# Performance work log

Hardware: AMD Instinct MI355X
Metric: run time of the kernel (lower is better)

## Reference

```python
import jax, jax.numpy as jnp
import numpy as np

N = 50000
E = 800000
D = 64


def setup_inputs() -> dict:
    key = jax.random.key(0)
    ks = jax.random.split(key, 6)
    s = 1.0 / np.sqrt(D)
    return {
        "x": jax.random.normal(ks[0], (N, D), dtype=jnp.float32),
        "edge_index": jax.random.randint(ks[1], (2, E), 0, N, dtype=jnp.int64),
        "W_l1": jax.random.normal(ks[2], (D, D), dtype=jnp.float32) * s,
        "b_l1": jnp.zeros((D,), dtype=jnp.float32),
        "W_r1": jax.random.normal(ks[3], (D, D), dtype=jnp.float32) * s,
        "W_l2": jax.random.normal(ks[4], (D, D), dtype=jnp.float32) * s,
        "b_l2": jnp.zeros((D,), dtype=jnp.float32),
        "W_r2": jax.random.normal(ks[5], (D, D), dtype=jnp.float32) * s,
    }


def _sage_conv(x, src, dst, W_l, b_l, W_r):
    # PyG SAGEConv (aggr='mean'): out = lin_l(mean_{j in N(i)} x_j) + lin_r(x_i)
    msgs = x[src]                                   # [E, D] gather
    agg = jax.ops.segment_sum(msgs, dst, num_segments=N)          # [N, D]
    cnt = jax.ops.segment_sum(jnp.ones((src.shape[0],), x.dtype), dst,
                              num_segments=N)                      # [N]
    agg = agg / jnp.maximum(cnt, 1.0)[:, None]       # mean with deg>=1 guard
    return agg @ W_l.T + b_l + x @ W_r.T


def reference(x, edge_index, W_l1, b_l1, W_r1, W_l2, b_l2, W_r2):
    src, dst = edge_index[0], edge_index[1]
    h = jnp.tanh(_sage_conv(x, src, dst, W_l1, b_l1, W_r1))
    out = _sage_conv(h, src, dst, W_l2, b_l2, W_r2)
    return out
```

## Files before the change

kernel.cpp:

```cpp
#include <hip/hip_runtime.h>
#include <hip/hip_bf16.h>

#define D 64

typedef __attribute__((ext_vector_type(8))) short bf16x8;
typedef __attribute__((ext_vector_type(4))) float f32x4;

__device__ __forceinline__ float bf2f(unsigned short u) {
    return __uint_as_float(((unsigned)u) << 16);
}
__device__ __forceinline__ unsigned short f2bf(float f) {
    __hip_bfloat16 b = __float2bfloat16(f);
    return *(unsigned short*)&b;
}


__global__ void prep_k(const float* __restrict__ x, unsigned short* __restrict__ xbf,
                       const float* __restrict__ Wl1, const float* __restrict__ Wr1,
                       const float* __restrict__ Wl2, const float* __restrict__ Wr2,
                       unsigned short* __restrict__ Wbf,
                       int* __restrict__ cnt, int n4, int ncnt4) {
    int i = blockIdx.x * blockDim.x + threadIdx.x;
    if (i < n4) {
        float4 v = ((const float4*)x)[i];
        ushort4 u;
        u.x = f2bf(v.x); u.y = f2bf(v.y); u.z = f2bf(v.z); u.w = f2bf(v.w);
        ((ushort4*)xbf)[i] = u;
    }
    if (i < ncnt4) ((int4*)cnt)[i] = make_int4(0, 0, 0, 0);
    if (i < 4096) {
        Wbf[i]           = f2bf(Wl1[i]);
        Wbf[4096 + i]    = f2bf(Wr1[i]);
        Wbf[8192 + i]    = f2bf(Wl2[i]);
        Wbf[12288 + i]   = f2bf(Wr2[i]);
    }
}


__global__ void pos_k(const int* __restrict__ dst, int* __restrict__ cnt,
                      unsigned short* __restrict__ pos, int E) {
    int e0 = (blockIdx.x * blockDim.x + threadIdx.x) * 4;
    if (e0 + 4 <= E) {
        int4 d = *(const int4*)(dst + e0);
        int px = atomicAdd(&cnt[d.x], 1);
        int py = atomicAdd(&cnt[d.y], 1);
        int pz = atomicAdd(&cnt[d.z], 1);
        int pw = atomicAdd(&cnt[d.w], 1);
        *(ushort4*)(pos + e0) = make_ushort4((unsigned short)px, (unsigned short)py,
                                             (unsigned short)pz, (unsigned short)pw);
    } else {
        for (int e = e0; e < E; ++e)
            pos[e] = (unsigned short)atomicAdd(&cnt[dst[e]], 1);
    }
}

__global__ void scanA_k(const int* __restrict__ cnt, int* __restrict__ rowptrL,
                        int* __restrict__ bsum, int N) {
    __shared__ int tmp[256];
    int gid = blockIdx.x * 256 + threadIdx.x;
    int v = (gid < N) ? cnt[gid] : 0;
    tmp[threadIdx.x] = v;
    __syncthreads();
    for (int off = 1; off < 256; off <<= 1) {
        int t = (threadIdx.x >= off) ? tmp[threadIdx.x - off] : 0;
        __syncthreads();
        tmp[threadIdx.x] += t;
        __syncthreads();
    }
    if (gid < N) rowptrL[gid] = tmp[threadIdx.x] - v;
    if (threadIdx.x == 255) bsum[blockIdx.x] = tmp[255];
}

__global__ void scanB_k(int* __restrict__ bsum, int nb) {
    __shared__ int tmp[256];
    int v = (threadIdx.x < nb) ? bsum[threadIdx.x] : 0;
    tmp[threadIdx.x] = v;
    __syncthreads();
    for (int off = 1; off < 256; off <<= 1) {
        int t = (threadIdx.x >= off) ? tmp[threadIdx.x - off] : 0;
        __syncthreads();
        tmp[threadIdx.x] += t;
        __syncthreads();
    }
    if (threadIdx.x < nb) bsum[threadIdx.x] = tmp[threadIdx.x] - v;
}

__global__ void fill2_k(const int* __restrict__ src, const int* __restrict__ dst,
                        const unsigned short* __restrict__ pos,
                        const int* __restrict__ rowptrL, const int* __restrict__ bsum,
                        unsigned short* __restrict__ col, int E) {
    int e0 = (blockIdx.x * blockDim.x + threadIdx.x) * 4;
    if (e0 + 4 <= E) {
        int4 d = *(const int4*)(dst + e0);
        int4 s = *(const int4*)(src + e0);
        ushort4 p = *(const ushort4*)(pos + e0);
        col[rowptrL[d.x] + bsum[d.x >> 8] + p.x] = (unsigned short)s.x;
        col[rowptrL[d.y] + bsum[d.y >> 8] + p.y] = (unsigned short)s.y;
        col[rowptrL[d.z] + bsum[d.z >> 8] + p.z] = (unsigned short)s.z;
        col[rowptrL[d.w] + bsum[d.w >> 8] + p.w] = (unsigned short)s.w;
    } else {
        for (int e = e0; e < E; ++e)
            col[rowptrL[dst[e]] + bsum[dst[e] >> 8] + pos[e]] = (unsigned short)src[e];
    }
}


__device__ __forceinline__ float tanh_fast(float v) {
    float e = __expf(2.f * v);
    return 1.f - 2.f * __builtin_amdgcn_rcpf(e + 1.f);
}

template <int TANH>
__global__ __launch_bounds__(256) void layer_k(
    const unsigned short* __restrict__ xb,
    const int* __restrict__ rowptrL, const int* __restrict__ bsum,
    const unsigned short* __restrict__ col,
    const unsigned short* __restrict__ Wlb,
    const unsigned short* __restrict__ Wrb,
    const float* __restrict__ bias,
    float* __restrict__ outf, unsigned short* __restrict__ outb, int N, int E)
{
    __shared__ unsigned short sagg[16][72];
    const int tid = threadIdx.x;
    const int idx = tid & 15;
    const int nl  = tid >> 4;
    const int n0  = blockIdx.x * 16;
    const int n   = n0 + nl;

    if (n < N) {
        const int beg = rowptrL[n] + bsum[n >> 8];
        const int end = (n + 1 < N) ? (rowptrL[n + 1] + bsum[(n + 1) >> 8]) : E;
        float ax[8], ay[8], az[8], aw[8];
        #pragma unroll
        for (int s = 0; s < 8; ++s) { ax[s]=0.f; ay[s]=0.f; az[s]=0.f; aw[s]=0.f; }
        for (int j = beg; j < end; j += 8) {
            #pragma unroll
            for (int s = 0; s < 8; ++s) {
                int jj = j + s;
                float m = (jj < end) ? 1.f : 0.f;
                jj = (jj < end) ? jj : end - 1;
                int c = col[jj];
                ushort4 u = *(const ushort4*)(xb + (size_t)c * D + idx * 4);
                ax[s] = fmaf(m, bf2f(u.x), ax[s]);
                ay[s] = fmaf(m, bf2f(u.y), ay[s]);
                az[s] = fmaf(m, bf2f(u.z), az[s]);
                aw[s] = fmaf(m, bf2f(u.w), aw[s]);
            }
        }
        float sx = ((ax[0]+ax[1])+(ax[2]+ax[3]))+((ax[4]+ax[5])+(ax[6]+ax[7]));
        float sy = ((ay[0]+ay[1])+(ay[2]+ay[3]))+((ay[4]+ay[5])+(ay[6]+ay[7]));
        float sz = ((az[0]+az[1])+(az[2]+az[3]))+((az[4]+az[5])+(az[6]+az[7]));
        float sw = ((aw[0]+aw[1])+(aw[2]+aw[3]))+((aw[4]+aw[5])+(aw[6]+aw[7]));
        const float inv = 1.0f / fmaxf((float)(end - beg), 1.0f);
        ushort4 o;
        o.x = f2bf(sx*inv); o.y = f2bf(sy*inv); o.z = f2bf(sz*inv); o.w = f2bf(sw*inv);
        *(ushort4*)&sagg[nl][idx * 4] = o;
    } else {
        *(ushort4*)&sagg[nl][idx * 4] = make_ushort4(0, 0, 0, 0);
    }
    __syncthreads();

    const int lane = tid & 63;
    const int wid  = tid >> 6;
    const int fr   = lane & 15;
    const int k0   = (lane >> 4) * 8;
    const int f    = wid * 16 + fr;

    bf16x8 bl[2], br[2];
    {
        const unsigned short* pl = Wlb + f * 64 + k0;
        const unsigned short* pr = Wrb + f * 64 + k0;
        #pragma unroll
        for (int kc = 0; kc < 2; ++kc) {
            bl[kc] = *(const bf16x8*)(pl + kc * 32);
            br[kc] = *(const bf16x8*)(pr + kc * 32);
        }
    }
    float bv = bias[f];
    f32x4 acc = (f32x4){bv, bv, bv, bv};

    bf16x8 aa[2], axf[2];
    #pragma unroll
    for (int kc = 0; kc < 2; ++kc)
        aa[kc] = *(const bf16x8*)&sagg[fr][kc * 32 + k0];
    {
        const unsigned short* px = xb + (size_t)(n0 + fr) * D + k0;
        #pragma unroll
        for (int kc = 0; kc < 2; ++kc)
            axf[kc] = *(const bf16x8*)(px + kc * 32);
    }

    #pragma unroll
    for (int kc = 0; kc < 2; ++kc) {
        acc = __builtin_amdgcn_mfma_f32_16x16x32_bf16(aa[kc],  bl[kc], acc, 0, 0, 0);
        acc = __builtin_amdgcn_mfma_f32_16x16x32_bf16(axf[kc], br[kc], acc, 0, 0, 0);
    }

    const int rbase = n0 + (lane >> 4) * 4;
    #pragma unroll
    for (int r = 0; r < 4; ++r) {
        int node = rbase + r;
        if (node < N) {
            float v = acc[r];
            if (TANH) {
                v = tanh_fast(v);
                outb[(size_t)node * D + f] = f2bf(v);
            } else {
                outf[(size_t)node * D + f] = v;
            }
        }
    }
}


extern "C" void kernel_launch(void* const* d_in, const int* in_sizes, int n_in,
                              void* d_out, int out_size, void* d_ws, size_t ws_size,
                              hipStream_t stream) {
    const float* x   = (const float*)d_in[0];
    const int*   ei  = (const int*)d_in[1];
    const float* Wl1 = (const float*)d_in[2];
    const float* bl1 = (const float*)d_in[3];
    const float* Wr1 = (const float*)d_in[4];
    const float* Wl2 = (const float*)d_in[5];
    const float* bl2 = (const float*)d_in[6];
    const float* Wr2 = (const float*)d_in[7];

    const int N = in_sizes[0] / D;
    const int E = in_sizes[1] / 2;
    const int* srcI = ei;
    const int* dstI = ei + E;

    auto al = [](size_t v) { return (v + 255) & ~(size_t)255; };
    char* w = (char*)d_ws;
    size_t off = 0;
    int*            cnt     = (int*)(w + off);            off += al((size_t)N * 4);
    int*            rowptrL = (int*)(w + off);            off += al((size_t)N * 4);
    int*            bsum    = (int*)(w + off);            off += al(1024);
    unsigned short* colA    = (unsigned short*)(w + off); off += al((size_t)E * 2);
    unsigned short* pos     = (unsigned short*)(w + off); off += al((size_t)E * 2);
    unsigned short* xbf     = (unsigned short*)(w + off); off += al((size_t)N * D * 2);
    unsigned short* hbf     = (unsigned short*)(w + off); off += al((size_t)N * D * 2);
    unsigned short* Wbf     = (unsigned short*)(w + off); off += al((size_t)4 * D * D * 2);
    unsigned short* Wb_l1 = Wbf, *Wb_r1 = Wbf + D*D, *Wb_l2 = Wbf + 2*D*D, *Wb_r2 = Wbf + 3*D*D;

    float* out = (float*)d_out;

    const int NB  = (N + 255) / 256;
    const int EB4 = (E / 4 + 255) / 256;
    const int PB  = (N * D / 4 + 255) / 256;
    const int LB  = (N + 15) / 16;

    prep_k<<<PB, 256, 0, stream>>>(x, xbf, Wl1, Wr1, Wl2, Wr2, Wbf,
                                   cnt, N * D / 4, (N + 3) / 4);
    pos_k<<<EB4, 256, 0, stream>>>(dstI, cnt, pos, E);
    scanA_k<<<NB, 256, 0, stream>>>(cnt, rowptrL, bsum, N);
    scanB_k<<<1, 256, 0, stream>>>(bsum, NB);
    fill2_k<<<EB4, 256, 0, stream>>>(srcI, dstI, pos, rowptrL, bsum, colA, E);

    layer_k<1><<<LB, 256, 0, stream>>>(xbf, rowptrL, bsum, colA, Wb_l1, Wb_r1, bl1,
                                       nullptr, hbf, N, E);
    layer_k<0><<<LB, 256, 0, stream>>>(hbf, rowptrL, bsum, colA, Wb_l2, Wb_r2, bl2,
                                       out, nullptr, N, E);
}
```

Before: 121.2 us.

## Split feature columns into two half-tables and aggregate each in separate passes

Stores bf16 node features as two 32-column halves. A new kernel aggregates the first half into a buffer, and the layer kernel aggregates the second half and combines both before the MFMA linear step. Each gather pass then touches a 3.2 MB table instead of 6.4 MB, aiming for better cache hit rates on the random neighbor gathers. The cost is an extra kernel launch per layer, a second walk over the column indices, and an extra write and read of the half-aggregate. The N bounds checks were also dropped, which is safe only because N is a multiple of 16.

```diff
diff --git a/kernel.cpp b/kernel.cpp
--- a/kernel.cpp
+++ b/kernel.cpp
@@ -15,7 +15,8 @@
 }
 
 
-__global__ void prep_k(const float* __restrict__ x, unsigned short* __restrict__ xbf,
+__global__ void prep_k(const float* __restrict__ x,
+                       unsigned short* __restrict__ xbA, unsigned short* __restrict__ xbB,
                        const float* __restrict__ Wl1, const float* __restrict__ Wr1,
                        const float* __restrict__ Wl2, const float* __restrict__ Wr2,
                        unsigned short* __restrict__ Wbf,
@@ -23,9 +24,11 @@
     int i = blockIdx.x * blockDim.x + threadIdx.x;
     if (i < n4) {
         float4 v = ((const float4*)x)[i];
+        int n = i >> 4, q = i & 15;
         ushort4 u;
         u.x = f2bf(v.x); u.y = f2bf(v.y); u.z = f2bf(v.z); u.w = f2bf(v.w);
-        ((ushort4*)xbf)[i] = u;
+        if (q < 8) *(ushort4*)(xbA + (size_t)n * 32 + q * 4) = u;
+        else       *(ushort4*)(xbB + (size_t)n * 32 + (q - 8) * 4) = u;
     }
     if (i < ncnt4) ((int4*)cnt)[i] = make_int4(0, 0, 0, 0);
     if (i < 4096) {
@@ -105,59 +108,102 @@
 }
 
 
+__global__ __launch_bounds__(256) void aggA_k(
+    const unsigned short* __restrict__ xbA,
+    const int* __restrict__ rowptrL, const int* __restrict__ bsum,
+    const unsigned short* __restrict__ col,
+    unsigned short* __restrict__ aggbA, int N, int E)
+{
+    const int tid = threadIdx.x;
+    const int idx = tid & 7;
+    const int n   = blockIdx.x * 32 + (tid >> 3);
+    if (n >= N) return;
+    const int beg = rowptrL[n] + bsum[n >> 8];
+    const int end = (n + 1 < N) ? (rowptrL[n + 1] + bsum[(n + 1) >> 8]) : E;
+
+    float ax[8], ay[8], az[8], aw[8];
+    #pragma unroll
+    for (int s = 0; s < 8; ++s) { ax[s]=0.f; ay[s]=0.f; az[s]=0.f; aw[s]=0.f; }
+    for (int j = beg; j < end; j += 8) {
+        #pragma unroll
+        for (int s = 0; s < 8; ++s) {
+            int jj = j + s;
+            float m = (jj < end) ? 1.f : 0.f;
+            jj = (jj < end) ? jj : end - 1;
+            int c = col[jj];
+            ushort4 u = *(const ushort4*)(xbA + (size_t)c * 32 + idx * 4);
+            ax[s] = fmaf(m, bf2f(u.x), ax[s]);
+            ay[s] = fmaf(m, bf2f(u.y), ay[s]);
+            az[s] = fmaf(m, bf2f(u.z), az[s]);
+            aw[s] = fmaf(m, bf2f(u.w), aw[s]);
+        }
+    }
+    float sx = ((ax[0]+ax[1])+(ax[2]+ax[3]))+((ax[4]+ax[5])+(ax[6]+ax[7]));
+    float sy = ((ay[0]+ay[1])+(ay[2]+ay[3]))+((ay[4]+ay[5])+(ay[6]+ay[7]));
+    float sz = ((az[0]+az[1])+(az[2]+az[3]))+((az[4]+az[5])+(az[6]+az[7]));
+    float sw = ((aw[0]+aw[1])+(aw[2]+aw[3]))+((aw[4]+aw[5])+(aw[6]+aw[7]));
+    const float inv = 1.0f / fmaxf((float)(end - beg), 1.0f);
+    ushort4 o;
+    o.x = f2bf(sx*inv); o.y = f2bf(sy*inv); o.z = f2bf(sz*inv); o.w = f2bf(sw*inv);
+    *(ushort4*)(aggbA + (size_t)n * 32 + idx * 4) = o;
+}
+
+
 __device__ __forceinline__ float tanh_fast(float v) {
     float e = __expf(2.f * v);
     return 1.f - 2.f * __builtin_amdgcn_rcpf(e + 1.f);
 }
 
 template <int TANH>
-__global__ __launch_bounds__(256) void layer_k(
-    const unsigned short* __restrict__ xb,
+__global__ __launch_bounds__(256) void layerB_k(
+    const unsigned short* __restrict__ xbA,
+    const unsigned short* __restrict__ xbB,
+    const unsigned short* __restrict__ aggbA,
     const int* __restrict__ rowptrL, const int* __restrict__ bsum,
     const unsigned short* __restrict__ col,
     const unsigned short* __restrict__ Wlb,
     const unsigned short* __restrict__ Wrb,
     const float* __restrict__ bias,
-    float* __restrict__ outf, unsigned short* __restrict__ outb, int N, int E)
+    float* __restrict__ outf,
+    unsigned short* __restrict__ houtA,
+    unsigned short* __restrict__ houtB,
+    int N, int E)
 {
     __shared__ unsigned short sagg[16][72];
     const int tid = threadIdx.x;
+    const int n0  = blockIdx.x * 16;
+
+    ushort4 aA;
+    if (tid < 128) aA = *(const ushort4*)(aggbA + (size_t)(n0 + (tid >> 3)) * 32 + (tid & 7) * 4);
+
     const int idx = tid & 15;
     const int nl  = tid >> 4;
-    const int n0  = blockIdx.x * 16;
     const int n   = n0 + nl;
-
-    if (n < N) {
-        const int beg = rowptrL[n] + bsum[n >> 8];
-        const int end = (n + 1 < N) ? (rowptrL[n + 1] + bsum[(n + 1) >> 8]) : E;
-        float ax[8], ay[8], az[8], aw[8];
+    const int beg = rowptrL[n] + bsum[n >> 8];
+    const int end = (n + 1 < N) ? (rowptrL[n + 1] + bsum[(n + 1) >> 8]) : E;
+    float ax[8], ay[8];
+    #pragma unroll
+    for (int s = 0; s < 8; ++s) { ax[s] = 0.f; ay[s] = 0.f; }
+    for (int j = beg; j < end; j += 8) {
         #pragma unroll
-        for (int s = 0; s < 8; ++s) { ax[s]=0.f; ay[s]=0.f; az[s]=0.f; aw[s]=0.f; }
-        for (int j = beg; j < end; j += 8) {
-            #pragma unroll
-            for (int s = 0; s < 8; ++s) {
-                int jj = j + s;
-                float m = (jj < end) ? 1.f : 0.f;
-                jj = (jj < end) ? jj : end - 1;
-                int c = col[jj];
-                ushort4 u = *(const ushort4*)(xb + (size_t)c * D + idx * 4);
-                ax[s] = fmaf(m, bf2f(u.x), ax[s]);
-                ay[s] = fmaf(m, bf2f(u.y), ay[s]);
-                az[s] = fmaf(m, bf2f(u.z), az[s]);
-                aw[s] = fmaf(m, bf2f(u.w), aw[s]);
-            }
+        for (int s = 0; s < 8; ++s) {
+            int jj = j + s;
+            float m = (jj < end) ? 1.f : 0.f;
+            jj = (jj < end) ? jj : end - 1;
+            int c = col[jj];
+            ushort2 u = *(const ushort2*)(xbB + (size_t)c * 32 + idx * 2);
+            ax[s] = fmaf(m, bf2f(u.x), ax[s]);
+            ay[s] = fmaf(m, bf2f(u.y), ay[s]);
         }
-        float sx = ((ax[0]+ax[1])+(ax[2]+ax[3]))+((ax[4]+ax[5])+(ax[6]+ax[7]));
-        float sy = ((ay[0]+ay[1])+(ay[2]+ay[3]))+((ay[4]+ay[5])+(ay[6]+ay[7]));
-        float sz = ((az[0]+az[1])+(az[2]+az[3]))+((az[4]+az[5])+(az[6]+az[7]));
-        float sw = ((aw[0]+aw[1])+(aw[2]+aw[3]))+((aw[4]+aw[5])+(aw[6]+aw[7]));
-        const float inv = 1.0f / fmaxf((float)(end - beg), 1.0f);
-        ushort4 o;
-        o.x = f2bf(sx*inv); o.y = f2bf(sy*inv); o.z = f2bf(sz*inv); o.w = f2bf(sw*inv);
-        *(ushort4*)&sagg[nl][idx * 4] = o;
-    } else {
-        *(ushort4*)&sagg[nl][idx * 4] = make_ushort4(0, 0, 0, 0);
-    }
+    }
+    float sx = ((ax[0]+ax[1])+(ax[2]+ax[3]))+((ax[4]+ax[5])+(ax[6]+ax[7]));
+    float sy = ((ay[0]+ay[1])+(ay[2]+ay[3]))+((ay[4]+ay[5])+(ay[6]+ay[7]));
+    const float inv = 1.0f / fmaxf((float)(end - beg), 1.0f);
+    ushort2 ob;
+    ob.x = f2bf(sx * inv); ob.y = f2bf(sy * inv);
+
+    if (tid < 128) *(ushort4*)&sagg[tid >> 3][(tid & 7) * 4] = aA;
+    *(ushort2*)&sagg[nl][32 + idx * 2] = ob;
     __syncthreads();
 
     const int lane = tid & 63;
@@ -180,15 +226,10 @@
     f32x4 acc = (f32x4){bv, bv, bv, bv};
 
     bf16x8 aa[2], axf[2];
-    #pragma unroll
-    for (int kc = 0; kc < 2; ++kc)
-        aa[kc] = *(const bf16x8*)&sagg[fr][kc * 32 + k0];
-    {
-        const unsigned short* px = xb + (size_t)(n0 + fr) * D + k0;
-        #pragma unroll
-        for (int kc = 0; kc < 2; ++kc)
-            axf[kc] = *(const bf16x8*)(px + kc * 32);
-    }
+    aa[0] = *(const bf16x8*)&sagg[fr][k0];
+    aa[1] = *(const bf16x8*)&sagg[fr][32 + k0];
+    axf[0] = *(const bf16x8*)(xbA + (size_t)(n0 + fr) * 32 + k0);
+    axf[1] = *(const bf16x8*)(xbB + (size_t)(n0 + fr) * 32 + k0);
 
     #pragma unroll
     for (int kc = 0; kc < 2; ++kc) {
@@ -200,14 +241,13 @@
     #pragma unroll
     for (int r = 0; r < 4; ++r) {
         int node = rbase + r;
-        if (node < N) {
-            float v = acc[r];
-            if (TANH) {
-                v = tanh_fast(v);
-                outb[(size_t)node * D + f] = f2bf(v);
-            } else {
-                outf[(size_t)node * D + f] = v;
-            }
+        float v = acc[r];
+        if (TANH) {
+            v = tanh_fast(v);
+            if (f < 32) houtA[(size_t)node * 32 + f]        = f2bf(v);
+            else        houtB[(size_t)node * 32 + (f - 32)] = f2bf(v);
+        } else {
+            outf[(size_t)node * D + f] = v;
         }
     }
 }
@@ -238,8 +278,11 @@
     int*            bsum    = (int*)(w + off);            off += al(1024);
     unsigned short* colA    = (unsigned short*)(w + off); off += al((size_t)E * 2);
     unsigned short* pos     = (unsigned short*)(w + off); off += al((size_t)E * 2);
-    unsigned short* xbf     = (unsigned short*)(w + off); off += al((size_t)N * D * 2);
-    unsigned short* hbf     = (unsigned short*)(w + off); off += al((size_t)N * D * 2);
+    unsigned short* xbA     = (unsigned short*)(w + off); off += al((size_t)N * 32 * 2);
+    unsigned short* xbB     = (unsigned short*)(w + off); off += al((size_t)N * 32 * 2);
+    unsigned short* hbA     = (unsigned short*)(w + off); off += al((size_t)N * 32 * 2);
+    unsigned short* hbB     = (unsigned short*)(w + off); off += al((size_t)N * 32 * 2);
+    unsigned short* aggbA   = (unsigned short*)(w + off); off += al((size_t)N * 32 * 2);
     unsigned short* Wbf     = (unsigned short*)(w + off); off += al((size_t)4 * D * D * 2);
     unsigned short* Wb_l1 = Wbf, *Wb_r1 = Wbf + D*D, *Wb_l2 = Wbf + 2*D*D, *Wb_r2 = Wbf + 3*D*D;
 
@@ -248,17 +291,20 @@
     const int NB  = (N + 255) / 256;
     const int EB4 = (E / 4 + 255) / 256;
     const int PB  = (N * D / 4 + 255) / 256;
+    const int GA  = (N + 31) / 32;
     const int LB  = (N + 15) / 16;
 
-    prep_k<<<PB, 256, 0, stream>>>(x, xbf, Wl1, Wr1, Wl2, Wr2, Wbf,
+    prep_k<<<PB, 256, 0, stream>>>(x, xbA, xbB, Wl1, Wr1, Wl2, Wr2, Wbf,
                                    cnt, N * D / 4, (N + 3) / 4);
     pos_k<<<EB4, 256, 0, stream>>>(dstI, cnt, pos, E);
     scanA_k<<<NB, 256, 0, stream>>>(cnt, rowptrL, bsum, N);
     scanB_k<<<1, 256, 0, stream>>>(bsum, NB);
     fill2_k<<<EB4, 256, 0, stream>>>(srcI, dstI, pos, rowptrL, bsum, colA, E);
 
-    layer_k<1><<<LB, 256, 0, stream>>>(xbf, rowptrL, bsum, colA, Wb_l1, Wb_r1, bl1,
-                                       nullptr, hbf, N, E);
-    layer_k<0><<<LB, 256, 0, stream>>>(hbf, rowptrL, bsum, colA, Wb_l2, Wb_r2, bl2,
-                                       out, nullptr, N, E);
-}
+    aggA_k<<<GA, 256, 0, stream>>>(xbA, rowptrL, bsum, colA, aggbA, N, E);
+    layerB_k<1><<<LB, 256, 0, stream>>>(xbA, xbB, aggbA, rowptrL, bsum, colA,
+                                        Wb_l1, Wb_r1, bl1, nullptr, hbA, hbB, N, E);
+    aggA_k<<<GA, 256, 0, stream>>>(hbA, rowptrL, bsum, colA, aggbA, N, E);
+    layerB_k<0><<<LB, 256, 0, stream>>>(hbA, hbB, aggbA, rowptrL, bsum, colA,
+                                        Wb_l2, Wb_r2, bl2, out, nullptr, nullptr, N, E);
+}
```

New measurement: 126.5 us. 4.4% more time.
